# Performance work log

Hardware: AMD Instinct MI355X
Metric: run time of the kernel (lower is better)

The kernel has to match this reference:

```python
import jax, jax.numpy as jnp
import numpy as np

NUM_ROT = 8
OUT_CH = 128
IN_CH = 128
KSIZE = 3


def _resample(filt, angle):
    """Rotate a (O, I, k, k) filter bank by `angle` via bilinear resampling,
    matching F.affine_grid/F.grid_sample with align_corners=True, zero padding."""
    k = filt.shape[-1]
    c, s = jnp.cos(angle), jnp.sin(angle)
    lin = jnp.linspace(-1.0, 1.0, k)
    gy, gx = jnp.meshgrid(lin, lin, indexing='ij')  # (k, k) output coords
    # theta = [[c, -s, 0], [s, c, 0]] applied to (x, y, 1)
    xs = c * gx - s * gy
    ys = s * gx + c * gy
    ix = (xs + 1.0) * 0.5 * (k - 1)  # normalized -> pixel coords
    iy = (ys + 1.0) * 0.5 * (k - 1)
    x0f, y0f = jnp.floor(ix), jnp.floor(iy)
    x0, y0 = x0f.astype(jnp.int32), y0f.astype(jnp.int32)
    wx, wy = ix - x0f, iy - y0f

    def tap(yi, xi, w):
        valid = ((yi >= 0) & (yi < k) & (xi >= 0) & (xi < k)).astype(filt.dtype)
        yc = jnp.clip(yi, 0, k - 1)
        xc = jnp.clip(xi, 0, k - 1)
        return filt[:, :, yc, xc] * (valid * w)  # (O, I, k, k)

    return (tap(y0, x0, (1 - wy) * (1 - wx)) + tap(y0, x0 + 1, (1 - wy) * wx)
            + tap(y0 + 1, x0, wy * (1 - wx)) + tap(y0 + 1, x0 + 1, wy * wx))


def setup_inputs() -> dict:
    key = jax.random.key(0)
    k1, k2, k3 = jax.random.split(key, 3)
    x = jax.random.normal(k1, (16, IN_CH, 128, 128), jnp.float32)
    # base_conv.weight: (out_channels * num_rotations, in_channels, k, k)
    weight = jax.random.normal(k2, (OUT_CH * NUM_ROT, IN_CH, KSIZE, KSIZE), jnp.float32) * 0.05
    rot_alpha = jax.random.normal(k3, (NUM_ROT,), jnp.float32) * 0.1 + 1.0
    return {"x": x, "weight": weight, "rot_alpha": rot_alpha}


def reference(x, weight, rot_alpha):
    R, O, K = NUM_ROT, OUT_CH, KSIZE
    # weight.view(O, R, I, K, K)[:, i] per rotation -> (R, O, I, K, K)
    w_r = weight.reshape(O, R, -1, K, K).transpose(1, 0, 2, 3, 4)
    angles = rot_alpha * (jnp.pi / 4) * jnp.arange(R, dtype=jnp.float32)
    rot_w = jax.vmap(_resample)(w_r, angles)  # (R, O, I, K, K)
    filters = rot_w.reshape(R * O, -1, K, K)
    # one conv with all rotated filter banks instead of R separate convs
    y = jax.lax.conv_general_dilated(
        x, filters, window_strides=(1, 1),
        padding=[(K // 2, K // 2), (K // 2, K // 2)],
        dimension_numbers=('NCHW', 'OIHW', 'NCHW'))  # (B, R*O, H, W)
    B, _, H, W = y.shape
    return y.reshape(B, R, O, H, W).max(axis=1)  # max over rotations
```

## Files before the change

### kernel.cpp

```cpp
#include <hip/hip_runtime.h>

typedef short short8 __attribute__((ext_vector_type(8)));
typedef float f32x4 __attribute__((ext_vector_type(4)));

#define XP_BYTES (16ull * 130 * 130 * 128 * 2)

static __device__ __forceinline__ unsigned short f2bf(float f) {
  unsigned u = __float_as_uint(f);
  u += 0x7FFFu + ((u >> 16) & 1u);
  return (unsigned short)(u >> 16);
}

static __device__ __forceinline__ void gload16(const void* g, void* l) {
  __builtin_amdgcn_global_load_lds(
      (const __attribute__((address_space(1))) void*)g,
      (__attribute__((address_space(3))) void*)l, 16, 0, 0);
}

static __device__ __forceinline__ float wtap(const float* f, int yi, int xi) {
  bool valid = (yi >= 0) & (yi < 3) & (xi >= 0) & (xi < 3);
  int yc = min(max(yi, 0), 2), xc = min(max(xi, 0), 2);
  return valid ? f[yc * 3 + xc] : 0.f;
}

__global__ __launch_bounds__(256) void wprep_kernel(
    const float* __restrict__ w, const float* __restrict__ rot_alpha,
    unsigned short* __restrict__ w2) {
  int gid = blockIdx.x * 256 + threadIdx.x;
  int ic = gid & 127;
  int nr = gid >> 7;
  int r = nr & 7;
  const float* wf = w + (size_t)nr * (128 * 9) + (size_t)ic * 9;
  float f[9];
#pragma unroll
  for (int q = 0; q < 9; ++q) f[q] = wf[q];
  float ang = rot_alpha[r] * 0.78539816339744830962f * (float)r;
  float sth, cth;
  sincosf(ang, &sth, &cth);
#pragma unroll
  for (int j = 0; j < 3; ++j) {
#pragma unroll
    for (int i = 0; i < 3; ++i) {
      float gy = (float)(j - 1), gx = (float)(i - 1);
      float xs = cth * gx - sth * gy;
      float ys = sth * gx + cth * gy;
      float ix = xs + 1.0f, iy = ys + 1.0f;
      float x0f = floorf(ix), y0f = floorf(iy);
      int x0 = (int)x0f, y0 = (int)y0f;
      float wx = ix - x0f, wy = iy - y0f;
      float acc = wtap(f, y0, x0) * (1.f - wy) * (1.f - wx)
                + wtap(f, y0, x0 + 1) * (1.f - wy) * wx
                + wtap(f, y0 + 1, x0) * wy * (1.f - wx)
                + wtap(f, y0 + 1, x0 + 1) * wy * wx;
      w2[(size_t)nr * 1152 + (size_t)(j * 3 + i) * 128 + ic] = f2bf(acc);
    }
  }
}

__global__ __launch_bounds__(256) void xprep_kernel(
    const float* __restrict__ x, unsigned short* __restrict__ xp) {
  const int yy = blockIdx.x;
  const int b = blockIdx.y;
  const int t = threadIdx.x;
  const size_t rowbase = ((size_t)b * 130 + yy) * (130 * 128);
  if (yy == 0 || yy == 129) {
    uint4 z = {0u, 0u, 0u, 0u};
    for (int i = t; i < 2080; i += 256)
      ((uint4*)(xp + rowbase))[i] = z;
    return;
  }
  const int y = yy - 1;
  __shared__ float lt[32][129];
  if (t < 32) {
    uint4 z = {0u, 0u, 0u, 0u};
    int xx = (t < 16) ? 0 : 129;
    int cc = (t & 15) * 8;
    *(uint4*)(xp + rowbase + (size_t)xx * 128 + cc) = z;
  }
  for (int c0 = 0; c0 < 128; c0 += 32) {
#pragma unroll
    for (int i = 0; i < 16; ++i) {
      int idx = i * 256 + t;
      int c = idx >> 7, wq = idx & 127;
      lt[c][wq] = x[(((size_t)b * 128 + c0 + c) * 128 + y) * 128 + wq];
    }
    __syncthreads();
#pragma unroll
    for (int i = 0; i < 2; ++i) {
      int u = i * 256 + t;
      int xx = u >> 2, cp = (u & 3) * 8;
      unsigned short v[8];
#pragma unroll
      for (int q = 0; q < 8; ++q) v[q] = f2bf(lt[cp + q][xx]);
      *(uint4*)(xp + rowbase + (size_t)(xx + 1) * 128 + c0 + cp) = *(uint4*)v;
    }
    __syncthreads();
  }
}

__global__ __launch_bounds__(256, 3) void conv_kernel(
    const unsigned short* __restrict__ xp,
    const unsigned short* __restrict__ w2,
    float* __restrict__ out) {
  __shared__ unsigned short lA[128 * 32];
  __shared__ unsigned short lB[128 * 32];
  __shared__ float lE[128 * 17];

  const int tid = threadIdx.x;
  const int lane = tid & 63;
  const int wv = tid >> 6;
  const int wr = wv >> 1;
  const int wc = wv & 1;

  const int nb = blockIdx.x;
  const int by = blockIdx.y;
  const int b = by >> 7;
  const int y = by & 127;

  f32x4 acc[4][4];
#pragma unroll
  for (int m = 0; m < 4; ++m)
#pragma unroll
    for (int n = 0; n < 4; ++n) acc[m][n] = (f32x4){0.f, 0.f, 0.f, 0.f};

  const int pixA = tid >> 2;
  const int cpA = (tid & 3) << 3;

  char* ldsAw = (char*)lA + wv * 1024;
  char* ldsBw = (char*)lB + wv * 1024;

  const size_t xrow0 = ((size_t)(b * 130 + y) * 130) * 128;
  const size_t bcol0 = (size_t)nb * 128 * 1152;

  for (int tap = 0; tap < 9; ++tap) {
    const int dy = tap / 3;
    const int dx = tap - dy * 3;
    const size_t abase = xrow0 + (size_t)dy * (130 * 128) + (size_t)dx * 128;
    const size_t bbase = bcol0 + (size_t)tap * 128;
#pragma unroll
    for (int cb = 0; cb < 4; ++cb) {
      const unsigned short* ga = xp + abase + cb * 32 + (size_t)pixA * 128 + cpA;
      const unsigned short* gb = w2 + bbase + cb * 32 + (size_t)pixA * 1152 + cpA;
      gload16(ga, ldsAw);
      gload16(ga + 64 * 128, ldsAw + 4096);
      gload16(gb, ldsBw);
      gload16(gb + 64 * 1152, ldsBw + 4096);
      __syncthreads();
      short8 af[4], bf[4];
      const int lrow = lane & 15;
      const int koff = (lane >> 4) << 3;
#pragma unroll
      for (int m = 0; m < 4; ++m)
        af[m] = *(const short8*)(lA + ((wr * 64 + m * 16 + lrow) * 32 + koff));
#pragma unroll
      for (int n = 0; n < 4; ++n)
        bf[n] = *(const short8*)(lB + ((wc * 64 + n * 16 + lrow) * 32 + koff));
#pragma unroll
      for (int m = 0; m < 4; ++m)
#pragma unroll
        for (int n = 0; n < 4; ++n)
          acc[m][n] = __builtin_amdgcn_mfma_f32_16x16x32_bf16(af[m], bf[n],
                                                              acc[m][n], 0, 0, 0);
      __syncthreads();
    }
  }

#pragma unroll
  for (int m = 0; m < 4; ++m)
#pragma unroll
    for (int n = 0; n < 4; ++n)
#pragma unroll
      for (int j = 0; j < 4; ++j) {
        float v = acc[m][n][j];
        v = fmaxf(v, __shfl_xor(v, 1, 64));
        v = fmaxf(v, __shfl_xor(v, 2, 64));
        v = fmaxf(v, __shfl_xor(v, 4, 64));
        if ((lane & 7) == 0) {
          int xx = wr * 64 + m * 16 + ((lane >> 4) << 2) + j;
          int ol = (wc * 64 + n * 16 + (lane & 15)) >> 3;
          lE[xx * 17 + ol] = v;
        }
      }
  __syncthreads();
  const size_t obase = (((size_t)b * 128 + nb * 16) * 128 + y) * 128;
#pragma unroll
  for (int i = 0; i < 8; ++i) {
    int idx = i * 256 + tid;
    int ol = idx >> 7;
    int xx = idx & 127;
    out[obase + (size_t)ol * (128 * 128) + xx] = lE[xx * 17 + ol];
  }
}

extern "C" void kernel_launch(void* const* d_in, const int* in_sizes, int n_in,
                              void* d_out, int out_size, void* d_ws, size_t ws_size,
                              hipStream_t stream) {
  const float* x = (const float*)d_in[0];
  const float* w = (const float*)d_in[1];
  const float* ra = (const float*)d_in[2];
  float* out = (float*)d_out;
  unsigned short* xp = (unsigned short*)d_ws;
  unsigned short* w2 = (unsigned short*)((char*)d_ws + XP_BYTES);

  hipLaunchKernelGGL(wprep_kernel, dim3(512), dim3(256), 0, stream, w, ra, w2);
  hipLaunchKernelGGL(xprep_kernel, dim3(130, 16), dim3(256), 0, stream, x, xp);
  hipLaunchKernelGGL(conv_kernel, dim3(8, 2048), dim3(256), 0, stream, xp, w2, out);
}
```

Before: 780.1 us.

## Enlarge conv tile to 256x256 with double-buffered swizzled LDS pipeline

The implicit-GEMM conv kernel now uses 512-thread blocks computing 256 pixels (two rows) by 256 output channels, with a K step of 64. Global-to-LDS loads are double-buffered and overlapped with MFMA work through explicit vmcnt waits. An XOR swizzle is added to cut LDS bank conflicts, s_setprio is raised around the MFMA bursts, and blocks are remapped for L2 locality. This reduces per-FLOP load and barrier overhead, at the cost of a large 128KB LDS footprint and high register pressure that may limit occupancy.

```diff
diff --git a/kernel.cpp b/kernel.cpp
--- a/kernel.cpp
+++ b/kernel.cpp
@@ -98,97 +98,140 @@
   }
 }
 
-__global__ __launch_bounds__(256, 3) void conv_kernel(
+__global__ __launch_bounds__(512, 2) void conv_kernel(
     const unsigned short* __restrict__ xp,
     const unsigned short* __restrict__ w2,
     float* __restrict__ out) {
-  __shared__ unsigned short lA[128 * 32];
-  __shared__ unsigned short lB[128 * 32];
-  __shared__ float lE[128 * 17];
+  __shared__ unsigned short lds[65536];
 
   const int tid = threadIdx.x;
   const int lane = tid & 63;
   const int wv = tid >> 6;
-  const int wr = wv >> 1;
-  const int wc = wv & 1;
-
-  const int nb = blockIdx.x;
-  const int by = blockIdx.y;
-  const int b = by >> 7;
-  const int y = by & 127;
-
-  f32x4 acc[4][4];
-#pragma unroll
-  for (int m = 0; m < 4; ++m)
-#pragma unroll
-    for (int n = 0; n < 4; ++n) acc[m][n] = (f32x4){0.f, 0.f, 0.f, 0.f};
-
-  const int pixA = tid >> 2;
-  const int cpA = (tid & 3) << 3;
-
-  char* ldsAw = (char*)lA + wv * 1024;
-  char* ldsBw = (char*)lB + wv * 1024;
-
-  const size_t xrow0 = ((size_t)(b * 130 + y) * 130) * 128;
-  const size_t bcol0 = (size_t)nb * 128 * 1152;
-
-  for (int tap = 0; tap < 9; ++tap) {
+  const int wr = wv >> 2;
+  const int wc = wv & 3;
+
+  const int bid = blockIdx.x;
+  const int wg = (bid & 7) * 512 + (bid >> 3);
+  const int mblk = wg >> 2;
+  const int nblk = wg & 3;
+  const int b = mblk >> 6;
+  const int y0 = (mblk & 63) << 1;
+
+  const int r0 = tid >> 3;
+  const int s0 = tid & 7;
+  const int wvoff = wv * 512;
+
+  const unsigned short* xbase = xp + (size_t)(b * 130 + y0) * 130 * 128;
+  const unsigned short* wbase = w2 + (size_t)nblk * 256 * 1152;
+
+  const int l15 = lane & 15;
+  const int lhi = lane >> 4;
+  const int swz = lhi ^ (l15 & 7);
+
+  f32x4 acc[8][4];
+#pragma unroll
+  for (int mf = 0; mf < 8; ++mf)
+#pragma unroll
+    for (int nf = 0; nf < 4; ++nf) acc[mf][nf] = (f32x4){0.f, 0.f, 0.f, 0.f};
+
+  auto stage = [&](int pb, int kt) {
+    const int tap = kt >> 1;
     const int dy = tap / 3;
     const int dx = tap - dy * 3;
-    const size_t abase = xrow0 + (size_t)dy * (130 * 128) + (size_t)dx * 128;
-    const size_t bbase = bcol0 + (size_t)tap * 128;
-#pragma unroll
-    for (int cb = 0; cb < 4; ++cb) {
-      const unsigned short* ga = xp + abase + cb * 32 + (size_t)pixA * 128 + cpA;
-      const unsigned short* gb = w2 + bbase + cb * 32 + (size_t)pixA * 1152 + cpA;
-      gload16(ga, ldsAw);
-      gload16(ga + 64 * 128, ldsAw + 4096);
-      gload16(gb, ldsBw);
-      gload16(gb + 64 * 1152, ldsBw + 4096);
-      __syncthreads();
-      short8 af[4], bf[4];
-      const int lrow = lane & 15;
-      const int koff = (lane >> 4) << 3;
-#pragma unroll
-      for (int m = 0; m < 4; ++m)
-        af[m] = *(const short8*)(lA + ((wr * 64 + m * 16 + lrow) * 32 + koff));
-#pragma unroll
-      for (int n = 0; n < 4; ++n)
-        bf[n] = *(const short8*)(lB + ((wc * 64 + n * 16 + lrow) * 32 + koff));
-#pragma unroll
-      for (int m = 0; m < 4; ++m)
-#pragma unroll
-        for (int n = 0; n < 4; ++n)
-          acc[m][n] = __builtin_amdgcn_mfma_f32_16x16x32_bf16(af[m], bf[n],
-                                                              acc[m][n], 0, 0, 0);
-      __syncthreads();
-    }
-  }
-
-#pragma unroll
-  for (int m = 0; m < 4; ++m)
-#pragma unroll
-    for (int n = 0; n < 4; ++n)
+    const int c0 = (kt & 1) << 6;
+    unsigned short* la = lds + pb * 16384;
+    unsigned short* lb = lds + 32768 + pb * 16384;
+#pragma unroll
+    for (int hp = 0; hp < 2; ++hp)
+#pragma unroll
+      for (int i = 0; i < 2; ++i) {
+        int r = i * 64 + r0;
+        int gs = s0 ^ (r & 7);
+        const unsigned short* ga =
+            xbase + ((size_t)((hp + dy) * 130) + r + dx) * 128 + c0 + gs * 8;
+        gload16(ga, la + hp * 8192 + i * 4096 + wvoff);
+      }
+#pragma unroll
+    for (int hn = 0; hn < 2; ++hn)
+#pragma unroll
+      for (int i = 0; i < 2; ++i) {
+        int r = i * 64 + r0;
+        int gs = s0 ^ (r & 7);
+        const unsigned short* gb =
+            wbase + (size_t)(hn * 128 + r) * 1152 + tap * 128 + c0 + gs * 8;
+        gload16(gb, lb + hn * 8192 + i * 4096 + wvoff);
+      }
+  };
+
+  stage(0, 0);
+
+#pragma unroll 2
+  for (int kt = 0; kt < 18; ++kt) {
+    const int pb = kt & 1;
+    if (kt < 17) {
+      stage(pb ^ 1, kt + 1);
+      asm volatile("s_waitcnt vmcnt(8)" ::: "memory");
+    } else {
+      asm volatile("s_waitcnt vmcnt(0)" ::: "memory");
+    }
+    __builtin_amdgcn_s_barrier();
+
+    const unsigned short* pA = lds + pb * 16384 + wr * 8192 + l15 * 64;
+    const unsigned short* pB =
+        lds + 32768 + pb * 16384 + (wc >> 1) * 8192 + (wc & 1) * 4096 + l15 * 64;
+#pragma unroll
+    for (int kk = 0; kk < 2; ++kk) {
+      const int sl = (swz ^ (kk << 2)) * 8;
+      short8 bf[4];
+#pragma unroll
+      for (int nf = 0; nf < 4; ++nf)
+        bf[nf] = *(const short8*)(pB + nf * 1024 + sl);
+#pragma unroll
+      for (int mh = 0; mh < 2; ++mh) {
+        short8 af[4];
+#pragma unroll
+        for (int q = 0; q < 4; ++q)
+          af[q] = *(const short8*)(pA + (mh * 4 + q) * 1024 + sl);
+        __builtin_amdgcn_s_setprio(1);
+#pragma unroll
+        for (int q = 0; q < 4; ++q)
+#pragma unroll
+          for (int nf = 0; nf < 4; ++nf)
+            acc[mh * 4 + q][nf] = __builtin_amdgcn_mfma_f32_16x16x32_bf16(
+                af[q], bf[nf], acc[mh * 4 + q][nf], 0, 0, 0);
+        __builtin_amdgcn_s_setprio(0);
+      }
+    }
+    __builtin_amdgcn_s_barrier();
+  }
+
+  float* lE = (float*)lds;
+#pragma unroll
+  for (int mf = 0; mf < 8; ++mf)
+#pragma unroll
+    for (int nf = 0; nf < 4; ++nf)
 #pragma unroll
       for (int j = 0; j < 4; ++j) {
-        float v = acc[m][n][j];
+        float v = acc[mf][nf][j];
         v = fmaxf(v, __shfl_xor(v, 1, 64));
         v = fmaxf(v, __shfl_xor(v, 2, 64));
         v = fmaxf(v, __shfl_xor(v, 4, 64));
         if ((lane & 7) == 0) {
-          int xx = wr * 64 + m * 16 + ((lane >> 4) << 2) + j;
-          int ol = (wc * 64 + n * 16 + (lane & 15)) >> 3;
-          lE[xx * 17 + ol] = v;
+          int pix = wr * 128 + mf * 16 + lhi * 4 + j;
+          int ol = wc * 8 + nf * 2 + ((lane >> 3) & 1);
+          lE[pix * 33 + ol] = v;
         }
       }
   __syncthreads();
-  const size_t obase = (((size_t)b * 128 + nb * 16) * 128 + y) * 128;
-#pragma unroll
-  for (int i = 0; i < 8; ++i) {
-    int idx = i * 256 + tid;
-    int ol = idx >> 7;
-    int xx = idx & 127;
-    out[obase + (size_t)ol * (128 * 128) + xx] = lE[xx * 17 + ol];
+  const size_t obase = ((size_t)(b * 128 + nblk * 32) * 128 + y0) * 128;
+#pragma unroll
+  for (int i = 0; i < 16; ++i) {
+    int idx = i * 512 + tid;
+    int ol = idx >> 8;
+    int pix = idx & 255;
+    int yl = pix >> 7;
+    int xx = pix & 127;
+    out[obase + (size_t)ol * 16384 + yl * 128 + xx] = lE[pix * 33 + ol];
   }
 }
 
@@ -204,5 +247,5 @@
 
   hipLaunchKernelGGL(wprep_kernel, dim3(512), dim3(256), 0, stream, w, ra, w2);
   hipLaunchKernelGGL(xprep_kernel, dim3(130, 16), dim3(256), 0, stream, x, xp);
-  hipLaunchKernelGGL(conv_kernel, dim3(8, 2048), dim3(256), 0, stream, xp, w2, out);
-}
+  hipLaunchKernelGGL(conv_kernel, dim3(4096), dim3(512), 0, stream, xp, w2, out);
+}
```

After: 756.2 us. 1.03x faster.

## Software-pipeline conv K-loop with double-buffered swizzled LDS and remapped grid

Applied to the files above, without the earlier changes.

Restructures the conv main loop into a double-buffered, software-pipelined schedule: async global-to-LDS loads for the next K slices are issued while MFMAs run on the current slice, with explicit vmcnt waits, raw s_barrier and setprio around the MFMA block. LDS rows are XOR-swizzled to cut bank conflicts on fragment reads, and the 2D grid becomes a 1D grid with a remapped block order so neighbouring blocks share weight/input tiles in cache. LDS use grows to 64KB and launch bounds drop to 2 blocks per CU, trading occupancy for latency hiding. Hand-placed wait counts risk subtle races if they are off.

```diff
diff --git a/kernel.cpp b/kernel.cpp
--- a/kernel.cpp
+++ b/kernel.cpp
@@ -98,13 +98,11 @@
   }
 }
 
-__global__ __launch_bounds__(256, 3) void conv_kernel(
+__global__ __launch_bounds__(256, 2) void conv_kernel(
     const unsigned short* __restrict__ xp,
     const unsigned short* __restrict__ w2,
     float* __restrict__ out) {
-  __shared__ unsigned short lA[128 * 32];
-  __shared__ unsigned short lB[128 * 32];
-  __shared__ float lE[128 * 17];
+  __shared__ unsigned short lds[32768];
 
   const int tid = threadIdx.x;
   const int lane = tid & 63;
@@ -112,83 +110,127 @@
   const int wr = wv >> 1;
   const int wc = wv & 1;
 
-  const int nb = blockIdx.x;
-  const int by = blockIdx.y;
-  const int b = by >> 7;
-  const int y = by & 127;
+  const int bid = blockIdx.x;
+  const int wg = (bid & 7) * 2048 + (bid >> 3);
+  const int mblk = wg >> 3;
+  const int nblk = wg & 7;
+  const int b = mblk >> 7;
+  const int y = mblk & 127;
+
+  const int r0 = tid >> 2;
+  const int s0 = tid & 3;
+  const int g0 = s0 ^ ((r0 >> 1) & 3);
+
+  const unsigned short* xpt =
+      xp + (size_t)(b * 130 + y) * 130 * 128 + r0 * 128 + g0 * 8;
+  const unsigned short* wpt =
+      w2 + (size_t)nblk * 128 * 1152 + (size_t)r0 * 1152 + g0 * 8;
+
+  const int l15 = lane & 15;
+  const int lhi = lane >> 4;
+  const int sa = (lhi ^ ((l15 >> 1) & 3)) * 8;
+
+  const int aRd = wr * 2048 + l15 * 32 + sa;
+  const int bRd = 16384 + wc * 2048 + l15 * 32 + sa;
 
   f32x4 acc[4][4];
 #pragma unroll
-  for (int m = 0; m < 4; ++m)
-#pragma unroll
-    for (int n = 0; n < 4; ++n) acc[m][n] = (f32x4){0.f, 0.f, 0.f, 0.f};
-
-  const int pixA = tid >> 2;
-  const int cpA = (tid & 3) << 3;
-
-  char* ldsAw = (char*)lA + wv * 1024;
-  char* ldsBw = (char*)lB + wv * 1024;
-
-  const size_t xrow0 = ((size_t)(b * 130 + y) * 130) * 128;
-  const size_t bcol0 = (size_t)nb * 128 * 1152;
-
-  for (int tap = 0; tap < 9; ++tap) {
-    const int dy = tap / 3;
-    const int dx = tap - dy * 3;
-    const size_t abase = xrow0 + (size_t)dy * (130 * 128) + (size_t)dx * 128;
-    const size_t bbase = bcol0 + (size_t)tap * 128;
-#pragma unroll
-    for (int cb = 0; cb < 4; ++cb) {
-      const unsigned short* ga = xp + abase + cb * 32 + (size_t)pixA * 128 + cpA;
-      const unsigned short* gb = w2 + bbase + cb * 32 + (size_t)pixA * 1152 + cpA;
-      gload16(ga, ldsAw);
-      gload16(ga + 64 * 128, ldsAw + 4096);
-      gload16(gb, ldsBw);
-      gload16(gb + 64 * 1152, ldsBw + 4096);
-      __syncthreads();
-      short8 af[4], bf[4];
-      const int lrow = lane & 15;
-      const int koff = (lane >> 4) << 3;
-#pragma unroll
-      for (int m = 0; m < 4; ++m)
-        af[m] = *(const short8*)(lA + ((wr * 64 + m * 16 + lrow) * 32 + koff));
-#pragma unroll
-      for (int n = 0; n < 4; ++n)
-        bf[n] = *(const short8*)(lB + ((wc * 64 + n * 16 + lrow) * 32 + koff));
-#pragma unroll
-      for (int m = 0; m < 4; ++m)
-#pragma unroll
-        for (int n = 0; n < 4; ++n)
-          acc[m][n] = __builtin_amdgcn_mfma_f32_16x16x32_bf16(af[m], bf[n],
-                                                              acc[m][n], 0, 0, 0);
-      __syncthreads();
-    }
-  }
-
-#pragma unroll
-  for (int m = 0; m < 4; ++m)
-#pragma unroll
-    for (int n = 0; n < 4; ++n)
+  for (int mf = 0; mf < 4; ++mf)
+#pragma unroll
+    for (int nf = 0; nf < 4; ++nf) acc[mf][nf] = (f32x4){0.f, 0.f, 0.f, 0.f};
+
+#define STAGE_A(BUF, HALF, KK, DY, DX, CH)                                    \
+  gload16(xpt + ((DY) * 130 + (HALF) * 64 + (DX)) * 128 + (CH) * 64 + (KK) * 32, \
+          lds + (BUF) * 8192 + (KK) * 4096 + (HALF) * 2048 + wv * 512)
+#define STAGE_B(BUF, HALF, KK, TAP, CH)                                       \
+  gload16(wpt + (size_t)(HALF) * 64 * 1152 + (TAP) * 128 + (CH) * 64 + (KK) * 32, \
+          lds + 16384 + (BUF) * 8192 + (KK) * 4096 + (HALF) * 2048 + wv * 512)
+
+#define VMW(n) asm volatile("s_waitcnt vmcnt(" #n ")" ::: "memory")
+#define LGKM0 asm volatile("s_waitcnt lgkmcnt(0)" ::: "memory")
+#define SCH0 __builtin_amdgcn_sched_barrier(0)
+
+#define STAGE_HALF(BUF, KK, T)                                                \
+  {                                                                           \
+    const int tp_ = (T) >> 1, c_ = (T) & 1;                                   \
+    const int dy_ = tp_ / 3, dx_ = tp_ - dy_ * 3;                             \
+    STAGE_A(BUF, 0, KK, dy_, dx_, c_);                                        \
+    STAGE_A(BUF, 1, KK, dy_, dx_, c_);                                        \
+    STAGE_B(BUF, 0, KK, tp_, c_);                                             \
+    STAGE_B(BUF, 1, KK, tp_, c_);                                             \
+  }
+
+#define PHASE(BUF, KK, STG, VMX)                                              \
+  {                                                                           \
+    const unsigned short* pA_ = lds + (BUF) * 8192 + (KK) * 4096 + aRd;       \
+    const unsigned short* pB_ = lds + (BUF) * 8192 + (KK) * 4096 + bRd;       \
+    short8 af[4], bf[4];                                                      \
+    _Pragma("unroll") for (int q = 0; q < 4; ++q)                             \
+        af[q] = *(const short8*)(pA_ + q * 512);                              \
+    _Pragma("unroll") for (int n = 0; n < 4; ++n)                             \
+        bf[n] = *(const short8*)(pB_ + n * 512);                              \
+    STG;                                                                      \
+    SCH0;                                                                     \
+    __builtin_amdgcn_s_barrier();                                             \
+    LGKM0;                                                                    \
+    __builtin_amdgcn_s_setprio(1);                                            \
+    _Pragma("unroll") for (int q = 0; q < 4; ++q)                             \
+        _Pragma("unroll") for (int n = 0; n < 4; ++n)                         \
+            acc[q][n] = __builtin_amdgcn_mfma_f32_16x16x32_bf16(              \
+                af[q], bf[n], acc[q][n], 0, 0, 0);                            \
+    __builtin_amdgcn_s_setprio(0);                                            \
+    VMX;                                                                      \
+    __builtin_amdgcn_s_barrier();                                             \
+  }
+
+  STAGE_HALF(0, 0, 0);
+  STAGE_HALF(0, 1, 0);
+  STAGE_HALF(1, 0, 1);
+  VMW(8);
+  SCH0;
+  __builtin_amdgcn_s_barrier();
+
+#pragma unroll 1
+  for (int kt = 0; kt < 16; ++kt) {
+    const int buf_ = kt & 1;
+    PHASE(buf_, 0, STAGE_HALF(buf_ ^ 1, 1, kt + 1), VMW(8));
+    PHASE(buf_, 1, STAGE_HALF(buf_, 0, kt + 2), VMW(8));
+  }
+  PHASE(0, 0, STAGE_HALF(1, 1, 17), VMW(8));
+  PHASE(0, 1, , VMW(4));
+  PHASE(1, 0, , VMW(0));
+  PHASE(1, 1, , VMW(0));
+
+#undef PHASE
+#undef STAGE_HALF
+#undef STAGE_A
+#undef STAGE_B
+
+  float* lE = (float*)lds;
+#pragma unroll
+  for (int mf = 0; mf < 4; ++mf)
+#pragma unroll
+    for (int nf = 0; nf < 4; ++nf)
 #pragma unroll
       for (int j = 0; j < 4; ++j) {
-        float v = acc[m][n][j];
+        float v = acc[mf][nf][j];
         v = fmaxf(v, __shfl_xor(v, 1, 64));
         v = fmaxf(v, __shfl_xor(v, 2, 64));
         v = fmaxf(v, __shfl_xor(v, 4, 64));
         if ((lane & 7) == 0) {
-          int xx = wr * 64 + m * 16 + ((lane >> 4) << 2) + j;
-          int ol = (wc * 64 + n * 16 + (lane & 15)) >> 3;
-          lE[xx * 17 + ol] = v;
+          int pix = wr * 64 + mf * 16 + lhi * 4 + j;
+          int ol = wc * 8 + nf * 2 + ((lane >> 3) & 1);
+          lE[pix * 17 + ol] = v;
         }
       }
   __syncthreads();
-  const size_t obase = (((size_t)b * 128 + nb * 16) * 128 + y) * 128;
+  const size_t obase = ((size_t)(b * 128 + nblk * 16) * 128 + y) * 128;
 #pragma unroll
   for (int i = 0; i < 8; ++i) {
     int idx = i * 256 + tid;
     int ol = idx >> 7;
     int xx = idx & 127;
-    out[obase + (size_t)ol * (128 * 128) + xx] = lE[xx * 17 + ol];
+    out[obase + (size_t)ol * 16384 + xx] = lE[xx * 17 + ol];
   }
 }
 
@@ -204,5 +246,5 @@
 
   hipLaunchKernelGGL(wprep_kernel, dim3(512), dim3(256), 0, stream, w, ra, w2);
   hipLaunchKernelGGL(xprep_kernel, dim3(130, 16), dim3(256), 0, stream, x, xp);
-  hipLaunchKernelGGL(conv_kernel, dim3(8, 2048), dim3(256), 0, stream, xp, w2, out);
-}
+  hipLaunchKernelGGL(conv_kernel, dim3(16384), dim3(256), 0, stream, xp, w2, out);
+}
```

Result: slower. 812.1 us (+4.1%).
